# Optimization experiments

Hardware: AMD Instinct MI355X
Metric: run time of the kernel (lower is better)

## Reference

```python
import jax, jax.numpy as jnp
import numpy as np
import math

EPS = 1e-6  # PCEN eps


def _logit(p):
    return math.log(p / (1.0 - p))


def _pcen(mel, log_s, log_alpha, log_delta, log_r, dmin, dmax):
    """PCEN: per-channel energy normalization. mel: (B, M, T); params: (M,)."""
    s = jnp.clip(jax.nn.sigmoid(log_s), 0.05, 0.3)            # (M,)
    alpha = jnp.clip(jax.nn.sigmoid(log_alpha), 0.9, 0.999)   # (M,)
    delta = jnp.clip(jnp.exp(log_delta), dmin, dmax)          # (M,)
    r = jnp.clip(jax.nn.sigmoid(log_r), 0.05, 0.25)           # (M,)

    # IIR smoother over time: smoother_0 = mel[..., 0];
    # for t in 0..T-1: smoother = (1-s)*smoother + s*mel_t  (t=0 included -> smoothed_0 = mel_0)
    mel_t = jnp.transpose(mel, (2, 0, 1))  # (T, B, M)

    def step(sm, x):
        sm = (1.0 - s) * sm + s * x
        return sm, sm

    _, smoothed_t = jax.lax.scan(step, mel_t[0], mel_t)
    smoothed = jnp.transpose(smoothed_t, (1, 2, 0))  # (B, M, T)

    gain = (EPS + smoothed) ** (-alpha[None, :, None])
    d = delta[None, :, None]
    rr = r[None, :, None]
    return (mel * gain + d) ** rr - d ** rr


def setup_inputs() -> dict:
    key = jax.random.key(0)
    B, M, T = 64, 80, 4000
    mel = jax.random.uniform(key, (B, M, T), dtype=jnp.float32)
    f = jnp.full
    return {
        "mel": mel,
        # non-stationary expert PCEN (s=0.025, alpha=0.99, delta=2.0, r=0.5)
        "log_s_ns": f((M,), _logit(0.025), jnp.float32),
        "log_alpha_ns": f((M,), _logit(0.99), jnp.float32),
        "log_delta_ns": f((M,), math.log(2.0), jnp.float32),
        "log_r_ns": f((M,), _logit(0.5), jnp.float32),
        # stationary expert PCEN (s=0.15, alpha=0.99, delta=0.01, r=0.1)
        "log_s_st": f((M,), _logit(0.15), jnp.float32),
        "log_alpha_st": f((M,), _logit(0.99), jnp.float32),
        "log_delta_st": f((M,), math.log(0.01), jnp.float32),
        "log_r_st": f((M,), _logit(0.1), jnp.float32),
        "gate_temp": jnp.asarray(5.0, jnp.float32),
    }


def reference(mel, log_s_ns, log_alpha_ns, log_delta_ns, log_r_ns,
              log_s_st, log_alpha_st, log_delta_st, log_r_st, gate_temp):
    out_ns = _pcen(mel, log_s_ns, log_alpha_ns, log_delta_ns, log_r_ns, 0.5, 5.0)
    out_st = _pcen(mel, log_s_st, log_alpha_st, log_delta_st, log_r_st, 0.001, 0.1)

    # routing signal: spectral flatness + spectral tilt (0 learnable params)
    log_mel = jnp.log(mel + 1e-8)
    geo = jnp.exp(jnp.mean(log_mel, axis=1, keepdims=True))          # (B,1,T)
    arith = jnp.mean(mel, axis=1, keepdims=True) + 1e-8
    sf = jnp.clip(geo / arith, 0.0, 1.0)

    M = mel.shape[1]
    low = jnp.mean(mel[:, : M // 3, :], axis=1, keepdims=True)
    high = jnp.mean(mel[:, 2 * M // 3 :, :], axis=1, keepdims=True)
    tilt = jnp.clip(low / (low + high + 1e-8), 0.0, 1.0)

    sf_adj = sf + (1.0 - sf) * jax.nn.relu(tilt - 0.6)
    gate = jax.nn.sigmoid(gate_temp * (sf_adj - 0.5))
    return gate * out_st + (1.0 - gate) * out_ns
```

## Files before the change

### kernel.cpp

```cpp
#include <hip/hip_runtime.h>
#include <math.h>

static constexpr int kM = 80;
static constexpr int kT = 4000;
static constexpr int kB = 64;
static constexpr int kLow = kM / 3;
static constexpr int kHighStart = 2 * kM / 3;
static constexpr int kHighCount = kM - kHighStart;
static constexpr int kC = 512;
static constexpr int kW = 256;
static constexpr int kE = 12;
static constexpr int kChunks = 8;
#define EPSF 1e-6f
#define LOG2E 1.4426950408889634f

typedef float vfloat4 __attribute__((ext_vector_type(4)));
typedef float vfloat2 __attribute__((ext_vector_type(2)));

__device__ __forceinline__ float hw_exp2(float x) { return __builtin_amdgcn_exp2f(x); }
__device__ __forceinline__ float hw_log2(float x) { return __builtin_amdgcn_logf(x); }

__device__ __forceinline__ float fast_sigmoid(float x) {
    return __builtin_amdgcn_rcpf(1.0f + hw_exp2(-x * LOG2E));
}

__global__ __launch_bounds__(512) void fused_kernel(
    const float* __restrict__ mel,
    const float* __restrict__ ls_ns, const float* __restrict__ la_ns,
    const float* __restrict__ ld_ns, const float* __restrict__ lr_ns,
    const float* __restrict__ ls_st, const float* __restrict__ la_st,
    const float* __restrict__ ld_st, const float* __restrict__ lr_st,
    const float* __restrict__ gate_temp,
    float* __restrict__ out)
{
    const int j   = blockIdx.x;
    const int b   = blockIdx.y;
    const int c0  = j * kC;
    const int tid = threadIdx.x;
    const int lane = tid & 63;
    const int wid  = tid >> 6;

    __shared__ float gate_s[kC];
    __shared__ vfloat4 prm[kM][3];

    if (tid < kM) {
        const int m = tid;
        const float s_ns     = fminf(fmaxf(fast_sigmoid(ls_ns[m]), 0.05f), 0.3f);
        const float alpha_ns = fminf(fmaxf(fast_sigmoid(la_ns[m]), 0.9f), 0.999f);
        const float delta_ns = fminf(fmaxf(hw_exp2(ld_ns[m] * LOG2E), 0.5f), 5.0f);
        const float r_ns     = fminf(fmaxf(fast_sigmoid(lr_ns[m]), 0.05f), 0.25f);
        const float s_st     = fminf(fmaxf(fast_sigmoid(ls_st[m]), 0.05f), 0.3f);
        const float alpha_st = fminf(fmaxf(fast_sigmoid(la_st[m]), 0.9f), 0.999f);
        const float delta_st = fminf(fmaxf(hw_exp2(ld_st[m] * LOG2E), 0.001f), 0.1f);
        const float r_st     = fminf(fmaxf(fast_sigmoid(lr_st[m]), 0.05f), 0.25f);
        vfloat4 w0; w0.x = 1.0f - s_ns; w0.y = 1.0f - s_st; w0.z = s_ns; w0.w = s_st;
        vfloat4 w1; w1.x = delta_ns; w1.y = delta_st; w1.z = -alpha_ns; w1.w = -alpha_st;
        vfloat4 w2; w2.x = r_ns; w2.y = r_st;
        w2.z = hw_exp2(r_ns * hw_log2(delta_ns));
        w2.w = hw_exp2(r_st * hw_log2(delta_st));
        prm[m][0] = w0; prm[m][1] = w1; prm[m][2] = w2;
    }

    {
        const int col = c0 + tid;
        if (col < kT) {
            const float* base = mel + (size_t)b * kM * kT + col;
            float slog = 0.f, ssum = 0.f, slow = 0.f, shigh = 0.f;
            #pragma unroll
            for (int m = 0; m < kM; ++m) {
                const float v = base[(size_t)m * kT];
                slog += hw_log2(v + 1e-8f);
                ssum += v;
                if (m < kLow)        slow  += v;
                if (m >= kHighStart) shigh += v;
            }
            const float geo   = hw_exp2(slog * (1.0f / kM));
            const float arith = ssum * (1.0f / kM) + 1e-8f;
            float sf = geo * __builtin_amdgcn_rcpf(arith);
            sf = fminf(fmaxf(sf, 0.0f), 1.0f);
            const float low  = slow  * (1.0f / kLow);
            const float high = shigh * (1.0f / kHighCount);
            float tilt = low * __builtin_amdgcn_rcpf(low + high + 1e-8f);
            tilt = fminf(fmaxf(tilt, 0.0f), 1.0f);
            const float sfa = sf + (1.0f - sf) * fmaxf(tilt - 0.6f, 0.0f);
            gate_s[tid] = fast_sigmoid(gate_temp[0] * (sfa - 0.5f));
        }
    }
    __syncthreads();

    const int ws = (j == 0) ? 0 : (c0 - kW);
    const int base_col = ws + lane * kE;
    const bool xvalid = (base_col + kE <= kT);

    for (int i = 0; i < 10; ++i) {
        const int m = wid * 10 + i;
        const vfloat4 w0 = prm[m][0];
        const vfloat4 w1 = prm[m][1];
        const vfloat4 w2 = prm[m][2];
        const vfloat2 a2 = {w0.x, w0.y};
        const vfloat2 s2 = {w0.z, w0.w};
        const vfloat2 d2 = {w1.x, w1.y};
        const float man = w1.z, mas = w1.w;
        const float r_ns = w2.x, r_st = w2.y, dr_ns = w2.z, dr_st = w2.w;
        const size_t rowoff = (size_t)(b * kM + m) * kT;

        float x[kE];
        if (xvalid) {
            const vfloat4* rp = reinterpret_cast<const vfloat4*>(mel + rowoff + base_col);
            #pragma unroll
            for (int q = 0; q < 3; ++q) {
                const vfloat4 v = rp[q];
                x[4*q+0] = v.x; x[4*q+1] = v.y; x[4*q+2] = v.z; x[4*q+3] = v.w;
            }
        } else {
            #pragma unroll
            for (int k = 0; k < kE; ++k) x[k] = 0.0f;
        }

        vfloat2 Bv = {0.0f, 0.0f};
        #pragma unroll
        for (int k = 0; k < kE; ++k) Bv = a2 * Bv + s2 * x[k];
        const vfloat2 p2 = a2 * a2;
        const vfloat2 p4 = p2 * p2;
        const vfloat2 p8 = p4 * p4;
        vfloat2 Av = p8 * p4;

        #pragma unroll
        for (int d = 1; d < 64; d <<= 1) {
            const float qAn = __shfl_up(Av.x, d);
            const float qAs = __shfl_up(Av.y, d);
            const float qBn = __shfl_up(Bv.x, d);
            const float qBs = __shfl_up(Bv.y, d);
            if (lane >= d) {
                const vfloat2 qA = {qAn, qAs};
                const vfloat2 qB = {qBn, qBs};
                Bv = Av * qB + Bv;
                Av = Av * qA;
            }
        }

        vfloat2 eA, eB;
        eA.x = __shfl_up(Av.x, 1); eA.y = __shfl_up(Av.y, 1);
        eB.x = __shfl_up(Bv.x, 1); eB.y = __shfl_up(Bv.y, 1);
        if (lane == 0) { eA = (vfloat2){1.0f, 1.0f}; eB = (vfloat2){0.0f, 0.0f}; }
        const float x0 = __shfl(x[0], 0);
        const vfloat2 v0 = {x0, x0};
        vfloat2 sm = eA * v0 + eB;

        #pragma unroll
        for (int q = 0; q < 3; ++q) {
            const int colq = base_col + 4 * q;
            const bool emit = (colq >= c0) && (colq < c0 + kC) && (colq < kT);
            vfloat4 g4 = {0.f, 0.f, 0.f, 0.f};
            if (emit) g4 = *reinterpret_cast<const vfloat4*>(gate_s + (colq - c0));
            vfloat4 r4;
            #pragma unroll
            for (int kk = 0; kk < 4; ++kk) {
                const float xv = x[4*q+kk];
                sm = a2 * sm + s2 * xv;
                if (emit) {
                    vfloat2 g2;
                    g2.x = hw_exp2(man * hw_log2(sm.x + EPSF));
                    g2.y = hw_exp2(mas * hw_log2(sm.y + EPSF));
                    const vfloat2 u2 = g2 * xv + d2;
                    const float on = hw_exp2(r_ns * hw_log2(u2.x)) - dr_ns;
                    const float os = hw_exp2(r_st * hw_log2(u2.y)) - dr_st;
                    r4[kk] = fmaf(g4[kk], os - on, on);
                }
            }
            if (emit) {
                *reinterpret_cast<vfloat4*>(out + rowoff + colq) = r4;
            }
        }
    }
}

extern "C" void kernel_launch(void* const* d_in, const int* in_sizes, int n_in,
                              void* d_out, int out_size, void* d_ws, size_t ws_size,
                              hipStream_t stream)
{
    const float* mel       = (const float*)d_in[0];
    const float* ls_ns     = (const float*)d_in[1];
    const float* la_ns     = (const float*)d_in[2];
    const float* ld_ns     = (const float*)d_in[3];
    const float* lr_ns     = (const float*)d_in[4];
    const float* ls_st     = (const float*)d_in[5];
    const float* la_st     = (const float*)d_in[6];
    const float* ld_st     = (const float*)d_in[7];
    const float* lr_st     = (const float*)d_in[8];
    const float* gate_temp = (const float*)d_in[9];
    float* out  = (float*)d_out;

    dim3 g(kChunks, kB);
    fused_kernel<<<g, 512, 0, stream>>>(mel, ls_ns, la_ns, ld_ns, lr_ns,
                                        ls_st, la_st, ld_st, lr_st,
                                        gate_temp, out);
}
```

Baseline: 187.2 us.

## Redistribute scanned PCEN values through LDS so all lanes do transcendental work

Halves the output chunk to 256 columns with a 256-column warm-up window, 8 elements per lane, and 256-thread blocks over a 16x64 grid. After the segmented IIR scan, each wave writes the smoothed states and inputs for its output columns to LDS. Each lane then reads back 4 contiguous columns and evaluates the log/exp-heavy PCEN and gate blend. Before, the lanes covering the warm-up region sat idle during that heavy phase. The routing-gate reduction is also split across 4 waves with vectorized loads and an LDS reduction. The trade-off is a larger share of redundant warm-up scanning per output and extra LDS traffic.

```diff
diff --git a/kernel.cpp b/kernel.cpp
--- a/kernel.cpp
+++ b/kernel.cpp
@@ -7,10 +7,11 @@
 static constexpr int kLow = kM / 3;
 static constexpr int kHighStart = 2 * kM / 3;
 static constexpr int kHighCount = kM - kHighStart;
-static constexpr int kC = 512;
+static constexpr int kC = 256;
 static constexpr int kW = 256;
-static constexpr int kE = 12;
-static constexpr int kChunks = 8;
+static constexpr int kWin = kC + kW;
+static constexpr int kE = 8;
+static constexpr int kChunks = 16;
 #define EPSF 1e-6f
 #define LOG2E 1.4426950408889634f
 
@@ -19,12 +20,11 @@
 
 __device__ __forceinline__ float hw_exp2(float x) { return __builtin_amdgcn_exp2f(x); }
 __device__ __forceinline__ float hw_log2(float x) { return __builtin_amdgcn_logf(x); }
-
 __device__ __forceinline__ float fast_sigmoid(float x) {
     return __builtin_amdgcn_rcpf(1.0f + hw_exp2(-x * LOG2E));
 }
 
-__global__ __launch_bounds__(512) void fused_kernel(
+__global__ __launch_bounds__(256, 4) void fused_kernel(
     const float* __restrict__ mel,
     const float* __restrict__ ls_ns, const float* __restrict__ la_ns,
     const float* __restrict__ ld_ns, const float* __restrict__ lr_ns,
@@ -33,15 +33,18 @@
     const float* __restrict__ gate_temp,
     float* __restrict__ out)
 {
-    const int j   = blockIdx.x;
-    const int b   = blockIdx.y;
-    const int c0  = j * kC;
-    const int tid = threadIdx.x;
+    const int j    = blockIdx.x;
+    const int b    = blockIdx.y;
+    const int c0   = j * kC;
+    const int tid  = threadIdx.x;
     const int lane = tid & 63;
     const int wid  = tid >> 6;
 
-    __shared__ float gate_s[kC];
+    __shared__ vfloat4 redu[4][4][64];
+    __shared__ float   gate_s[kC];
     __shared__ vfloat4 prm[kM][3];
+    __shared__ vfloat2 c_sm[4][kE][32];
+    __shared__ float   c_x[4][kE][32];
 
     if (tid < kM) {
         const int m = tid;
@@ -62,28 +65,59 @@
     }
 
     {
-        const int col = c0 + tid;
-        if (col < kT) {
-            const float* base = mel + (size_t)b * kM * kT + col;
-            float slog = 0.f, ssum = 0.f, slow = 0.f, shigh = 0.f;
-            #pragma unroll
-            for (int m = 0; m < kM; ++m) {
-                const float v = base[(size_t)m * kT];
-                slog += hw_log2(v + 1e-8f);
+        const int qcol = c0 + 4 * lane;
+        vfloat4 slog = {0.f,0.f,0.f,0.f}, ssum = {0.f,0.f,0.f,0.f};
+        vfloat4 slow = {0.f,0.f,0.f,0.f}, shigh = {0.f,0.f,0.f,0.f};
+        if (qcol < kT) {
+            const float* base = mel + (size_t)b * kM * kT + qcol;
+            const int m0 = wid * 20;
+            #pragma unroll
+            for (int jj = 0; jj < 20; ++jj) {
+                const int m = m0 + jj;
+                const vfloat4 v = *reinterpret_cast<const vfloat4*>(base + (size_t)m * kT);
+                vfloat4 lg;
+                lg.x = hw_log2(v.x + 1e-8f); lg.y = hw_log2(v.y + 1e-8f);
+                lg.z = hw_log2(v.z + 1e-8f); lg.w = hw_log2(v.w + 1e-8f);
+                slog += lg;
                 ssum += v;
                 if (m < kLow)        slow  += v;
                 if (m >= kHighStart) shigh += v;
             }
-            const float geo   = hw_exp2(slog * (1.0f / kM));
-            const float arith = ssum * (1.0f / kM) + 1e-8f;
-            float sf = geo * __builtin_amdgcn_rcpf(arith);
-            sf = fminf(fmaxf(sf, 0.0f), 1.0f);
-            const float low  = slow  * (1.0f / kLow);
-            const float high = shigh * (1.0f / kHighCount);
-            float tilt = low * __builtin_amdgcn_rcpf(low + high + 1e-8f);
-            tilt = fminf(fmaxf(tilt, 0.0f), 1.0f);
-            const float sfa = sf + (1.0f - sf) * fmaxf(tilt - 0.6f, 0.0f);
-            gate_s[tid] = fast_sigmoid(gate_temp[0] * (sfa - 0.5f));
+        }
+        redu[wid][0][lane] = slog;
+        redu[wid][1][lane] = ssum;
+        redu[wid][2][lane] = slow;
+        redu[wid][3][lane] = shigh;
+    }
+    __syncthreads();
+
+    if (wid == 0) {
+        const int qcol = c0 + 4 * lane;
+        if (qcol < kT) {
+            const vfloat4 slog  = redu[0][0][lane] + redu[1][0][lane] + redu[2][0][lane] + redu[3][0][lane];
+            const vfloat4 ssum  = redu[0][1][lane] + redu[1][1][lane] + redu[2][1][lane] + redu[3][1][lane];
+            const vfloat4 slow  = redu[0][2][lane] + redu[1][2][lane] + redu[2][2][lane] + redu[3][2][lane];
+            const vfloat4 shigh = redu[0][3][lane] + redu[1][3][lane] + redu[2][3][lane] + redu[3][3][lane];
+            const float gt = gate_temp[0];
+            const float sl[4] = {slog.x, slog.y, slog.z, slog.w};
+            const float ss[4] = {ssum.x, ssum.y, ssum.z, ssum.w};
+            const float lo[4] = {slow.x, slow.y, slow.z, slow.w};
+            const float hi[4] = {shigh.x, shigh.y, shigh.z, shigh.w};
+            vfloat4 o;
+            #pragma unroll
+            for (int q = 0; q < 4; ++q) {
+                const float geo   = hw_exp2(sl[q] * (1.0f / kM));
+                const float arith = ss[q] * (1.0f / kM) + 1e-8f;
+                float sf = geo * __builtin_amdgcn_rcpf(arith);
+                sf = fminf(fmaxf(sf, 0.0f), 1.0f);
+                const float low  = lo[q] * (1.0f / kLow);
+                const float high = hi[q] * (1.0f / kHighCount);
+                float tilt = low * __builtin_amdgcn_rcpf(low + high + 1e-8f);
+                tilt = fminf(fmaxf(tilt, 0.0f), 1.0f);
+                const float sfa = sf + (1.0f - sf) * fmaxf(tilt - 0.6f, 0.0f);
+                o[q] = fast_sigmoid(gt * (sfa - 0.5f));
+            }
+            *reinterpret_cast<vfloat4*>(gate_s + 4 * lane) = o;
         }
     }
     __syncthreads();
@@ -91,9 +125,11 @@
     const int ws = (j == 0) ? 0 : (c0 - kW);
     const int base_col = ws + lane * kE;
     const bool xvalid = (base_col + kE <= kT);
-
-    for (int i = 0; i < 10; ++i) {
-        const int m = wid * 10 + i;
+    const int col4 = c0 + 4 * lane;
+    const bool dvalid = (col4 < kT);
+
+    for (int i = 0; i < 20; ++i) {
+        const int m = wid * 20 + i;
         const vfloat4 w0 = prm[m][0];
         const vfloat4 w1 = prm[m][1];
         const vfloat4 w2 = prm[m][2];
@@ -107,11 +143,10 @@
         float x[kE];
         if (xvalid) {
             const vfloat4* rp = reinterpret_cast<const vfloat4*>(mel + rowoff + base_col);
-            #pragma unroll
-            for (int q = 0; q < 3; ++q) {
-                const vfloat4 v = rp[q];
-                x[4*q+0] = v.x; x[4*q+1] = v.y; x[4*q+2] = v.z; x[4*q+3] = v.w;
-            }
+            const vfloat4 v0q = rp[0];
+            const vfloat4 v1q = rp[1];
+            x[0] = v0q.x; x[1] = v0q.y; x[2] = v0q.z; x[3] = v0q.w;
+            x[4] = v1q.x; x[5] = v1q.y; x[6] = v1q.z; x[7] = v1q.w;
         } else {
             #pragma unroll
             for (int k = 0; k < kE; ++k) x[k] = 0.0f;
@@ -122,8 +157,7 @@
         for (int k = 0; k < kE; ++k) Bv = a2 * Bv + s2 * x[k];
         const vfloat2 p2 = a2 * a2;
         const vfloat2 p4 = p2 * p2;
-        const vfloat2 p8 = p4 * p4;
-        vfloat2 Av = p8 * p4;
+        vfloat2 Av = p4 * p4;
 
         #pragma unroll
         for (int d = 1; d < 64; d <<= 1) {
@@ -148,29 +182,32 @@
         vfloat2 sm = eA * v0 + eB;
 
         #pragma unroll
-        for (int q = 0; q < 3; ++q) {
-            const int colq = base_col + 4 * q;
-            const bool emit = (colq >= c0) && (colq < c0 + kC) && (colq < kT);
-            vfloat4 g4 = {0.f, 0.f, 0.f, 0.f};
-            if (emit) g4 = *reinterpret_cast<const vfloat4*>(gate_s + (colq - c0));
+        for (int k = 0; k < kE; ++k) {
+            sm = a2 * sm + s2 * x[k];
+            const int e = base_col + k - c0;
+            if (e >= 0 && e < kC) {
+                c_sm[wid][e & 7][e >> 3] = sm;
+                c_x[wid][e & 7][e >> 3]  = x[k];
+            }
+        }
+
+        if (dvalid) {
+            const vfloat4 g4 = *reinterpret_cast<const vfloat4*>(gate_s + 4 * lane);
             vfloat4 r4;
             #pragma unroll
             for (int kk = 0; kk < 4; ++kk) {
-                const float xv = x[4*q+kk];
-                sm = a2 * sm + s2 * xv;
-                if (emit) {
-                    vfloat2 g2;
-                    g2.x = hw_exp2(man * hw_log2(sm.x + EPSF));
-                    g2.y = hw_exp2(mas * hw_log2(sm.y + EPSF));
-                    const vfloat2 u2 = g2 * xv + d2;
-                    const float on = hw_exp2(r_ns * hw_log2(u2.x)) - dr_ns;
-                    const float os = hw_exp2(r_st * hw_log2(u2.y)) - dr_st;
-                    r4[kk] = fmaf(g4[kk], os - on, on);
-                }
-            }
-            if (emit) {
-                *reinterpret_cast<vfloat4*>(out + rowoff + colq) = r4;
-            }
+                const int e = 4 * lane + kk;
+                const vfloat2 smv = c_sm[wid][e & 7][e >> 3];
+                const float  xv   = c_x[wid][e & 7][e >> 3];
+                vfloat2 g2;
+                g2.x = hw_exp2(man * hw_log2(smv.x + EPSF));
+                g2.y = hw_exp2(mas * hw_log2(smv.y + EPSF));
+                const vfloat2 u2 = g2 * xv + d2;
+                const float on = hw_exp2(r_ns * hw_log2(u2.x)) - dr_ns;
+                const float os = hw_exp2(r_st * hw_log2(u2.y)) - dr_st;
+                r4[kk] = fmaf(g4[kk], os - on, on);
+            }
+            *reinterpret_cast<vfloat4*>(out + rowoff + col4) = r4;
         }
     }
 }
@@ -192,7 +229,7 @@
     float* out  = (float*)d_out;
 
     dim3 g(kChunks, kB);
-    fused_kernel<<<g, 512, 0, stream>>>(mel, ls_ns, la_ns, ld_ns, lr_ns,
+    fused_kernel<<<g, 256, 0, stream>>>(mel, ls_ns, la_ns, ld_ns, lr_ns,
                                         ls_st, la_st, ld_st, lr_st,
                                         gate_temp, out);
 }
```

After: 199.9 us. 6.8% more time.
